# Kernel tuning notes

Hardware: AMD Instinct MI355X
Metric: run time of the kernel (lower is better)

The kernel has to match this reference:

```python
import jax, jax.numpy as jnp
import numpy as np
from jax import lax

U, K, POOL, STRIDE, FC = 300, 19, 7, 7, 100   # num_units, filter size, maxpool, fc_size
B, L, D = 256, 1000, 4                        # batch, seq len, DNA dim
P = (L - (K - 1) - (POOL - 1) - 1) // STRIDE + 1  # post_pool_size = 140
EPS = 1e-5  # BatchNorm eps (eval mode with running stats; Dropout is identity in eval)


def setup_inputs() -> dict:
    key = jax.random.key(0)
    ks = jax.random.split(key, 24)
    rn = lambda k, shp, s=0.1: jax.random.normal(k, shp, jnp.float32) * s
    return {
        "input_seq": jax.random.normal(ks[0], (B, L, D), jnp.float32),
        # per-unit conv (groups=U on tiled input == plain Conv1d(4, U, K))
        "w_conv": rn(ks[1], (U, D, K)), "b_conv": rn(ks[2], (U,)),
        "g1": 1.0 + rn(ks[3], (U,)), "be1": rn(ks[4], (U,)),
        "m1": rn(ks[5], (U,)), "v1": 1.0 + jax.random.uniform(ks[6], (U,), jnp.float32),
        # per-unit FC1 (grouped 1x1 conv: P -> FC per unit)
        "w_fc1": rn(ks[7], (U, FC, P)), "b_fc1": rn(ks[8], (U, FC)),
        "g2": 1.0 + rn(ks[9], (U, FC)), "be2": rn(ks[10], (U, FC)),
        "m2": rn(ks[11], (U, FC)), "v2": 1.0 + jax.random.uniform(ks[12], (U, FC), jnp.float32),
        # per-unit FC2 (grouped 1x1 conv: FC -> 1 per unit)
        "w_fc2": rn(ks[13], (U, FC)), "b_fc2": rn(ks[14], (U,)),
        "g3": 1.0 + rn(ks[15], (U,)), "be3": rn(ks[16], (U,)),
        "m3": rn(ks[17], (U,)), "v3": 1.0 + jax.random.uniform(ks[18], (U,), jnp.float32),
        # final Linear(U, 1)
        "w_out": rn(ks[19], (U, 1)), "b_out": rn(ks[20], (1,)),
    }


def reference(input_seq, w_conv, b_conv, g1, be1, m1, v1, w_fc1, b_fc1,
              g2, be2, m2, v2, w_fc2, b_fc2, g3, be3, m3, v3, w_out, b_out):
    x = jnp.transpose(input_seq, (0, 2, 1))  # B,D,L
    # grouped conv on input tiled U times: every group sees the same D=4 channels,
    # so it is exactly a plain Conv1d(D, U, K).
    conv = lax.conv_general_dilated(
        x, w_conv, (1,), 'VALID', dimension_numbers=('NCH', 'OIH', 'NCH')
    ) + b_conv[None, :, None]                 # B,U,L' (L'=L-K+1)
    a = (conv - m1[None, :, None]) * (g1 / jnp.sqrt(v1 + EPS))[None, :, None] + be1[None, :, None]
    a = jnp.exp(a)
    pooled = lax.reduce_window(a, -jnp.inf, lax.max,
                               (1, 1, POOL), (1, 1, STRIDE), 'VALID')  # B,U,P
    # Flatten->Unsqueeze->grouped 1x1 conv == per-unit matmul over P
    h = jnp.einsum('bup,ufp->buf', pooled, w_fc1) + b_fc1               # B,U,FC
    h = jax.nn.relu((h - m2) * (g2 / jnp.sqrt(v2 + EPS)) + be2)
    z = jnp.einsum('buf,uf->bu', h, w_fc2) + b_fc2                      # B,U
    z = jax.nn.relu((z - m3) * (g3 / jnp.sqrt(v3 + EPS)) + be3)
    return jax.nn.sigmoid(z @ w_out + b_out)                            # B,1
```

## Files before the change

### kernel.cpp

```cpp
#include <hip/hip_runtime.h>
#include <hip/hip_bf16.h>
#include <math.h>

#define U_   300
#define K_   19
#define FC_  100
#define B_   256
#define L_   1000
#define P_   140
#define EPS_ 1e-5f
#define WLD_ 144

typedef unsigned short ushort_t;
typedef __attribute__((ext_vector_type(8)))  short short8v;
typedef __attribute__((ext_vector_type(16))) float f32x16;

__device__ __forceinline__ ushort_t f2bf(float f) {
    union { float f; unsigned u; } a; a.f = f;
    unsigned r = a.u + 0x7fffu + ((a.u >> 16) & 1u);
    return (ushort_t)(r >> 16);
}

__global__ __launch_bounds__(256, 4)
void pack_conv_k(const float* __restrict__ w_conv, const float* __restrict__ b_conv,
                 const float* __restrict__ g1, const float* __restrict__ be1,
                 const float* __restrict__ m1, const float* __restrict__ v1,
                 ushort_t* __restrict__ w_bf, float* __restrict__ o1g)
{
    const int t = blockIdx.x * 256 + threadIdx.x;
    if (t < 320 * 80) {
        const int u = t / 80, j = t - u * 80;
        float val = 0.f;
        if (u < U_ && j < 76) {
            const int tp = j >> 2;
            const int d  = j & 3;
            const float s1 = g1[u] / sqrtf(v1[u] + EPS_);
            val = w_conv[u * 76 + 19 * d + tp] * s1;
        }
        const int nt = u >> 5, r = u & 31;
        const int kc = j >> 4, rem = j & 15;
        const int half = rem >> 3, e = rem & 7;
        w_bf[nt * 2560 + kc * 512 + half * 256 + r * 8 + e] = f2bf(val);
    }
    if (t < 320) {
        float o = 0.f;
        if (t < U_) {
            const float s1 = g1[t] / sqrtf(v1[t] + EPS_);
            o = (b_conv[t] - m1[t]) * s1 + be1[t];
        }
        o1g[t] = o;
    }
}

__global__ __launch_bounds__(256, 6)
void conv_mfma_k(const float4* __restrict__ x4,
                 const ushort_t* __restrict__ w_bf,
                 const float* __restrict__ o1g,
                 ushort_t* __restrict__ pooled)
{
    __shared__ ushort_t xls[544];
    __shared__ ushort_t stage[32][18];
    const int tid = threadIdx.x;
    const int bx  = blockIdx.x;
    const int nh  = blockIdx.y;
    const int b   = blockIdx.z;
    const int w0  = bx * 16;
    const int l0  = w0 * 7;

    if (tid < 136) {
        const int gi = l0 + tid;
        float4 v = make_float4(0.f, 0.f, 0.f, 0.f);
        if (gi < L_) v = x4[(size_t)b * L_ + gi];
        ushort4 pk4;
        pk4.x = f2bf(v.x); pk4.y = f2bf(v.y); pk4.z = f2bf(v.z); pk4.w = f2bf(v.w);
        *(ushort4*)&xls[4 * tid] = pk4;
    }
    __syncthreads();

    const int lane = tid & 63;
    const int wv   = tid >> 6;
    const int half = lane >> 5;
    const int r32  = lane & 31;

    const int sreg = (r32 & 3) + 4 * (r32 >> 3);
    const int sh   = (r32 >> 2) & 1;
    const int off  = sreg < 7  ? sreg + 7 * sh
                   : sreg < 14 ? sreg + 7 + 7 * sh
                               : 28 + (sreg - 14) + 2 * sh;

    const char* xb = (const char*)xls + 8 * (28 * wv + off) + 16 * half;

    short8v aA[5];
#pragma unroll
    for (int kc = 0; kc < 5; ++kc)
        aA[kc] = *(const short8v*)(xb + 32 * kc);

    const char* wgl = (const char*)w_bf + nh * 5 * 5120 + 16 * lane;

    const int p0off = 4 * wv + half;

    for (int ntp = 0; ntp < 5; ++ntp) {
        short8v bfr[5];
#pragma unroll
        for (int kc = 0; kc < 5; ++kc)
            bfr[kc] = *(const short8v*)(wgl + ntp * 5120 + kc * 1024);
        const int ubase = nh * 160 + ntp * 32;
        const float o1u = o1g[ubase + r32];

        f32x16 acc = {};
#pragma unroll
        for (int kc = 0; kc < 5; ++kc)
            acc = __builtin_amdgcn_mfma_f32_32x32x16_bf16(aA[kc], bfr[kc], acc, 0, 0, 0);

        float m0 = acc[0], m1 = acc[7];
#pragma unroll
        for (int j = 1; j < 7; ++j)  m0 = fmaxf(m0, acc[j]);
#pragma unroll
        for (int j = 8; j < 14; ++j) m1 = fmaxf(m1, acc[j]);

        stage[r32][p0off]     = f2bf(__expf(m0 + o1u));
        stage[r32][p0off + 2] = f2bf(__expf(m1 + o1u));
        __syncthreads();

        if (tid < 128) {
            const int du = tid >> 2, dc = tid & 3;
            const int ug = ubase + du;
            const int wq = w0 + 4 * dc;
            if (ug < U_ && wq + 3 < P_) {
                const ushort4 st = *(const ushort4*)&stage[du][4 * dc];
                *(ushort4*)&pooled[((size_t)ug * B_ + b) * P_ + wq] = st;
            }
        }
        __syncthreads();
    }
}

__global__ __launch_bounds__(256, 3)
void fc_mfma_k(const ushort_t* __restrict__ pooled,
               const float* __restrict__ w_fc1,
               const float* __restrict__ b_fc1,
               const float* __restrict__ g2,
               const float* __restrict__ be2,
               const float* __restrict__ m2,
               const float* __restrict__ v2,
               const float* __restrict__ w_fc2,
               const float* __restrict__ b_fc2,
               const float* __restrict__ g3,
               const float* __restrict__ be3,
               const float* __restrict__ m3,
               const float* __restrict__ v3,
               float* __restrict__ zT)
{
    __shared__ ushort_t wlds[FC_ * WLD_];
    __shared__ float zred[128][33];
    const int tid  = threadIdx.x;
    const int bid = blockIdx.x;
    int u, bt;
    if (bid < 592) {
        const int r = bid & 7, k = bid >> 3;
        bt = k & 1;
        u  = (k >> 1) * 8 + r;
    } else {
        const int t = bid - 592;
        u  = 296 + (t >> 1);
        bt = t & 1;
    }

    const int lane = tid & 63;
    const int wv   = tid >> 6;
    const int half = lane >> 5;
    const int r32  = lane & 31;

    const int brow = bt * 128 + wv * 32 + r32;
    const ushort_t* __restrict__ abase =
        pooled + ((size_t)u * B_ + brow) * P_ + half * 8;
    short8v a[9];
#pragma unroll
    for (int kc = 0; kc < 9; ++kc)
        a[kc] = *(const short8v*)(abase + kc * 16);

    const float* __restrict__ wsrc = w_fc1 + (size_t)u * FC_ * P_;
    for (int idx = tid; idx < FC_ * 35; idx += 256) {
        const int f = idx / 35, j = idx - f * 35;
        const float4 v = *(const float4*)(wsrc + f * P_ + 4 * j);
        ushort4 pk;
        pk.x = f2bf(v.x); pk.y = f2bf(v.y); pk.z = f2bf(v.z); pk.w = f2bf(v.w);
        *(ushort4*)&wlds[f * WLD_ + 4 * j] = pk;
    }
    for (int idx = tid; idx < FC_ * 4; idx += 256) {
        const int f = idx >> 2, k = 140 + (idx & 3);
        wlds[f * WLD_ + k] = 0;
    }
    __syncthreads();

    const ushort_t* __restrict__ bl0 = &wlds[r32 * WLD_ + half * 8];
    const ushort_t* __restrict__ bl1 = &wlds[(32 + r32) * WLD_ + half * 8];
    const ushort_t* __restrict__ bl2 = &wlds[(64 + r32) * WLD_ + half * 8];
    const int f3c = (96 + r32 < FC_) ? (96 + r32) : (FC_ - 1);
    const ushort_t* __restrict__ bl3 = &wlds[f3c * WLD_ + half * 8];

    f32x16 acc0 = {}, acc1 = {}, acc2 = {}, acc3 = {};
#pragma unroll
    for (int kc = 0; kc < 9; ++kc) {
        const short8v b0 = *(const short8v*)(bl0 + kc * 16);
        const short8v b1 = *(const short8v*)(bl1 + kc * 16);
        const short8v b2 = *(const short8v*)(bl2 + kc * 16);
        const short8v b3 = *(const short8v*)(bl3 + kc * 16);
        acc0 = __builtin_amdgcn_mfma_f32_32x32x16_bf16(a[kc], b0, acc0, 0, 0, 0);
        acc1 = __builtin_amdgcn_mfma_f32_32x32x16_bf16(a[kc], b1, acc1, 0, 0, 0);
        acc2 = __builtin_amdgcn_mfma_f32_32x32x16_bf16(a[kc], b2, acc2, 0, 0, 0);
        acc3 = __builtin_amdgcn_mfma_f32_32x32x16_bf16(a[kc], b3, acc3, 0, 0, 0);
    }

    float s2[4], o2[4], w2[4];
#pragma unroll
    for (int n = 0; n < 4; ++n) {
        const int f = n * 32 + r32;
        if (f < FC_) {
            const int fg = u * FC_ + f;
            const float ss = g2[fg] / sqrtf(v2[fg] + EPS_);
            s2[n] = ss;
            o2[n] = (b_fc1[fg] - m2[fg]) * ss + be2[fg];
            w2[n] = w_fc2[fg];
        } else {
            s2[n] = 0.f; o2[n] = 0.f; w2[n] = 0.f;
        }
    }
#pragma unroll
    for (int rg = 0; rg < 16; ++rg) {
        const int row = (rg & 3) + 8 * (rg >> 2) + 4 * half;
        float s = fmaxf(fmaf(acc0[rg], s2[0], o2[0]), 0.f) * w2[0];
        s = fmaf(fmaxf(fmaf(acc1[rg], s2[1], o2[1]), 0.f), w2[1], s);
        s = fmaf(fmaxf(fmaf(acc2[rg], s2[2], o2[2]), 0.f), w2[2], s);
        s = fmaf(fmaxf(fmaf(acc3[rg], s2[3], o2[3]), 0.f), w2[3], s);
        zred[wv * 32 + row][r32] = s;
    }
    __syncthreads();

    if (tid < 128) {
        float s = 0.f;
#pragma unroll
        for (int j = 0; j < 32; ++j) s += zred[tid][j];
        const float s3 = g3[u] / sqrtf(v3[u] + EPS_);
        const float o3 = (b_fc2[u] - m3[u]) * s3 + be3[u];
        zT[(size_t)(bt * 128 + tid) * 304 + u] = fmaxf(fmaf(s, s3, o3), 0.f);
    }
}

__global__ __launch_bounds__(64, 8)
void out_k(const float* __restrict__ zT,
           const float* __restrict__ w_out,
           const float* __restrict__ b_out,
           float* __restrict__ out)
{
    const int lane = threadIdx.x;
    const int b    = blockIdx.x;
    const float4* zr = (const float4*)(zT + (size_t)b * 304);
    const float4* w4 = (const float4*)w_out;

    float s = 0.f;
    for (int i = lane; i < 75; i += 64) {
        const float4 z = zr[i], w = w4[i];
        s += z.x * w.x + z.y * w.y + z.z * w.z + z.w * w.w;
    }
#pragma unroll
    for (int o = 32; o > 0; o >>= 1) s += __shfl_xor(s, o);
    if (lane == 0)
        out[b] = 1.0f / (1.0f + __expf(-(s + b_out[0])));
}

extern "C" void kernel_launch(void* const* d_in, const int* in_sizes, int n_in,
                              void* d_out, int out_size, void* d_ws, size_t ws_size,
                              hipStream_t stream)
{
    const float* input_seq = (const float*)d_in[0];
    const float* w_conv    = (const float*)d_in[1];
    const float* b_conv    = (const float*)d_in[2];
    const float* g1        = (const float*)d_in[3];
    const float* be1       = (const float*)d_in[4];
    const float* m1        = (const float*)d_in[5];
    const float* v1        = (const float*)d_in[6];
    const float* w_fc1     = (const float*)d_in[7];
    const float* b_fc1     = (const float*)d_in[8];
    const float* g2        = (const float*)d_in[9];
    const float* be2       = (const float*)d_in[10];
    const float* m2        = (const float*)d_in[11];
    const float* v2        = (const float*)d_in[12];
    const float* w_fc2     = (const float*)d_in[13];
    const float* b_fc2     = (const float*)d_in[14];
    const float* g3        = (const float*)d_in[15];
    const float* be3       = (const float*)d_in[16];
    const float* m3        = (const float*)d_in[17];
    const float* v3        = (const float*)d_in[18];
    const float* w_out     = (const float*)d_in[19];
    const float* b_out     = (const float*)d_in[20];

    char* p = (char*)d_ws;
    ushort_t* pooled = (ushort_t*)p;   p += (size_t)B_ * U_ * P_ * 2;
    ushort_t* w_bf   = (ushort_t*)p;   p += 320 * 80 * 2;
    float*    o1g    = (float*)p;      p += 320 * 4;
    float*    zT     = (float*)p;      p += (size_t)B_ * 304 * 4;

    pack_conv_k<<<dim3(100), 256, 0, stream>>>(
        w_conv, b_conv, g1, be1, m1, v1, w_bf, o1g);

    conv_mfma_k<<<dim3(9, 2, B_), 256, 0, stream>>>(
        (const float4*)input_seq, w_bf, o1g, pooled);

    fc_mfma_k<<<dim3(600), 256, 0, stream>>>(
        pooled, w_fc1, b_fc1, g2, be2, m2, v2, w_fc2, b_fc2,
        g3, be3, m3, v3, zT);

    out_k<<<dim3(B_), 64, 0, stream>>>(zT, w_out, b_out, (float*)d_out);
}
```

Before: 53.25 us.

## Process four batch rows per conv block to reuse loaded weight fragments

The conv kernel now handles four batch elements per block, loading each weight B-fragment once and issuing four independent MFMA chains against it. Input tiles for all four batches are staged in shared memory, and the pooled-output staging buffer is widened so one store pass writes all four batches. This cuts redundant weight global loads and per-block overhead, and gives more MFMA work per barrier. In exchange it uses more registers (occupancy hint lowered from 6 to 4) and launches a quarter as many blocks.

```diff
diff --git a/kernel.cpp b/kernel.cpp
--- a/kernel.cpp
+++ b/kernel.cpp
@@ -52,28 +52,29 @@
     }
 }
 
-__global__ __launch_bounds__(256, 6)
+__global__ __launch_bounds__(256, 4)
 void conv_mfma_k(const float4* __restrict__ x4,
                  const ushort_t* __restrict__ w_bf,
                  const float* __restrict__ o1g,
                  ushort_t* __restrict__ pooled)
 {
-    __shared__ ushort_t xls[544];
-    __shared__ ushort_t stage[32][18];
+    __shared__ ushort_t xls[4][544];
+    __shared__ ushort_t stage[32][66];
     const int tid = threadIdx.x;
     const int bx  = blockIdx.x;
     const int nh  = blockIdx.y;
-    const int b   = blockIdx.z;
+    const int b0  = 4 * blockIdx.z;
     const int w0  = bx * 16;
     const int l0  = w0 * 7;
 
-    if (tid < 136) {
-        const int gi = l0 + tid;
+    for (int i = tid; i < 544; i += 256) {
+        const int bat = i / 136, row = i - bat * 136;
+        const int gi = l0 + row;
         float4 v = make_float4(0.f, 0.f, 0.f, 0.f);
-        if (gi < L_) v = x4[(size_t)b * L_ + gi];
+        if (gi < L_) v = x4[(size_t)(b0 + bat) * L_ + gi];
         ushort4 pk4;
         pk4.x = f2bf(v.x); pk4.y = f2bf(v.y); pk4.z = f2bf(v.z); pk4.w = f2bf(v.w);
-        *(ushort4*)&xls[4 * tid] = pk4;
+        *(ushort4*)&xls[bat][4 * row] = pk4;
     }
     __syncthreads();
 
@@ -88,12 +89,11 @@
                    : sreg < 14 ? sreg + 7 + 7 * sh
                                : 28 + (sreg - 14) + 2 * sh;
 
-    const char* xb = (const char*)xls + 8 * (28 * wv + off) + 16 * half;
-
-    short8v aA[5];
-#pragma unroll
-    for (int kc = 0; kc < 5; ++kc)
-        aA[kc] = *(const short8v*)(xb + 32 * kc);
+    const int xoffb = 8 * (28 * wv + off) + 16 * half;
+    const char* xb0 = (const char*)&xls[0][0] + xoffb;
+    const char* xb1 = (const char*)&xls[1][0] + xoffb;
+    const char* xb2 = (const char*)&xls[2][0] + xoffb;
+    const char* xb3 = (const char*)&xls[3][0] + xoffb;
 
     const char* wgl = (const char*)w_bf + nh * 5 * 5120 + 16 * lane;
 
@@ -107,28 +107,47 @@
         const int ubase = nh * 160 + ntp * 32;
         const float o1u = o1g[ubase + r32];
 
-        f32x16 acc = {};
-#pragma unroll
-        for (int kc = 0; kc < 5; ++kc)
-            acc = __builtin_amdgcn_mfma_f32_32x32x16_bf16(aA[kc], bfr[kc], acc, 0, 0, 0);
-
-        float m0 = acc[0], m1 = acc[7];
-#pragma unroll
-        for (int j = 1; j < 7; ++j)  m0 = fmaxf(m0, acc[j]);
-#pragma unroll
-        for (int j = 8; j < 14; ++j) m1 = fmaxf(m1, acc[j]);
-
-        stage[r32][p0off]     = f2bf(__expf(m0 + o1u));
-        stage[r32][p0off + 2] = f2bf(__expf(m1 + o1u));
+        f32x16 acc0 = {}, acc1 = {}, acc2 = {}, acc3 = {};
+#pragma unroll
+        for (int kc = 0; kc < 5; ++kc) {
+            const short8v a0 = *(const short8v*)(xb0 + 32 * kc);
+            const short8v a1 = *(const short8v*)(xb1 + 32 * kc);
+            const short8v a2 = *(const short8v*)(xb2 + 32 * kc);
+            const short8v a3 = *(const short8v*)(xb3 + 32 * kc);
+            acc0 = __builtin_amdgcn_mfma_f32_32x32x16_bf16(a0, bfr[kc], acc0, 0, 0, 0);
+            acc1 = __builtin_amdgcn_mfma_f32_32x32x16_bf16(a1, bfr[kc], acc1, 0, 0, 0);
+            acc2 = __builtin_amdgcn_mfma_f32_32x32x16_bf16(a2, bfr[kc], acc2, 0, 0, 0);
+            acc3 = __builtin_amdgcn_mfma_f32_32x32x16_bf16(a3, bfr[kc], acc3, 0, 0, 0);
+        }
+
+#define POOL_STORE(ACC, BAT)                                                   \
+        {                                                                      \
+            float m0 = ACC[0], m1 = ACC[7];                                    \
+            _Pragma("unroll")                                                  \
+            for (int j = 1; j < 7; ++j)  m0 = fmaxf(m0, ACC[j]);               \
+            _Pragma("unroll")                                                  \
+            for (int j = 8; j < 14; ++j) m1 = fmaxf(m1, ACC[j]);               \
+            stage[r32][(BAT) * 16 + p0off]     = f2bf(__expf(m0 + o1u));       \
+            stage[r32][(BAT) * 16 + p0off + 2] = f2bf(__expf(m1 + o1u));       \
+        }
+        POOL_STORE(acc0, 0)
+        POOL_STORE(acc1, 1)
+        POOL_STORE(acc2, 2)
+        POOL_STORE(acc3, 3)
+#undef POOL_STORE
         __syncthreads();
 
-        if (tid < 128) {
-            const int du = tid >> 2, dc = tid & 3;
-            const int ug = ubase + du;
-            const int wq = w0 + 4 * dc;
-            if (ug < U_ && wq + 3 < P_) {
-                const ushort4 st = *(const ushort4*)&stage[du][4 * dc];
-                *(ushort4*)&pooled[((size_t)ug * B_ + b) * P_ + wq] = st;
+#pragma unroll
+        for (int it = 0; it < 2; ++it) {
+            const int idx = tid + 256 * it;
+            const int du  = idx >> 4;
+            const int bat = (idx >> 2) & 3;
+            const int dc  = idx & 3;
+            const int ug  = ubase + du;
+            const int wq  = w0 + 4 * dc;
+            if (ug < U_ && wq + 4 <= P_) {
+                const ushort4 st = *(const ushort4*)&stage[du][bat * 16 + 4 * dc];
+                *(ushort4*)&pooled[((size_t)ug * B_ + (b0 + bat)) * P_ + wq] = st;
             }
         }
         __syncthreads();
@@ -304,7 +323,7 @@
     pack_conv_k<<<dim3(100), 256, 0, stream>>>(
         w_conv, b_conv, g1, be1, m1, v1, w_bf, o1g);
 
-    conv_mfma_k<<<dim3(9, 2, B_), 256, 0, stream>>>(
+    conv_mfma_k<<<dim3(9, 2, B_ / 4), 256, 0, stream>>>(
         (const float4*)input_seq, w_bf, o1g, pooled);
 
     fc_mfma_k<<<dim3(600), 256, 0, stream>>>(
```

New measurement: 89.94 us. 1.69x slower.
